# Kernel optimization log

Hardware: AMD Instinct MI355X
Metric: run time of the kernel (lower is better)

The kernel has to match this reference:

```python
import jax, jax.numpy as jnp
import numpy as np

# FP4 E2M1 lookup table: low 3 bits = magnitude code, bit 3 = sign
E2M1_LUT = jnp.array([0.0, 0.5, 1.0, 1.5, 2.0, 3.0, 4.0, 6.0,
                      -0.0, -0.5, -1.0, -1.5, -2.0, -3.0, -4.0, -6.0],
                     dtype=jnp.float32)

INNER_BLOCK = 16    # elements per fp8 (e4m3) inner scale
OUTER_BLOCK = 128   # elements per fp32 outlier scale


def dequant_fp4(w_q, w_os, w_is):
    """Dequantize packed FP4 weights.
    w_q : [out, in//2] int (uint8 semantics: two nibbles per byte)
    w_os: [out, in//128] fp32 outlier scales
    w_is: [out, in//16]  fp32 values on the fp8 e4m3 grid (inner scales)
    returns W: [out, in] fp32
    """
    out_f = w_q.shape[0]
    lo = E2M1_LUT[w_q & 0xF]          # even in-feature indices
    hi = E2M1_LUT[(w_q >> 4) & 0xF]   # odd in-feature indices
    w = jnp.stack([lo, hi], axis=-1).reshape(out_f, -1)  # [out, in]
    w = w * jnp.repeat(w_is, INNER_BLOCK, axis=1)
    w = w * jnp.repeat(w_os, OUTER_BLOCK, axis=1)
    return w


def setup_inputs() -> dict:
    key = jax.random.key(0)
    k1, k2, k3, k4 = jax.random.split(key, 4)
    M, IN, OUT = 8192, 4096, 16384

    x = jax.random.normal(k1, (M, IN), dtype=jnp.float32)

    # packed FP4 codes (uint8 semantics, stored as int32 for portability)
    w_q = jax.random.randint(k2, (OUT, IN // 2), 0, 256, dtype=jnp.int32)

    # per-128-block fp32 outlier scales (positive)
    w_os = jax.random.uniform(k3, (OUT, IN // OUTER_BLOCK), dtype=jnp.float32,
                              minval=0.001, maxval=0.01)

    # per-16-block inner scales, snapped to the fp8 e4m3 grid
    w_is_raw = jax.random.uniform(k4, (OUT, IN // INNER_BLOCK), dtype=jnp.float32,
                                  minval=0.25, maxval=2.0)
    w_is = w_is_raw.astype(jnp.float8_e4m3fn).astype(jnp.float32)

    # transposed dequantized weight, exactly consistent (used by backward)
    w_t = dequant_fp4(w_q, w_os, w_is).T  # [IN, OUT]

    return {"x": x, "w_q": w_q, "w_os": w_os, "w_is": w_is, "w_t": w_t}


def reference(x, w_q, w_os, w_is, w_t):
    # x.float() + flatten-to-2D already satisfied by setup (x is [M, in] fp32).
    w = dequant_fp4(w_q, w_os, w_is)          # [out, in]
    y = jnp.einsum('mk,nk->mn', x, w)         # fused dequant + GEMM math
    return y
```

## Files before the change

kernel.cpp:

```cpp
#include <hip/hip_runtime.h>
#include <hip/hip_bf16.h>
#include <stdint.h>
#include <stddef.h>

#define M_DIM 8192
#define K_DIM 4096
#define N_DIM 16384

#define BM 256
#define BN 256
#define BK 64
#define KT (K_DIM / BK)
#define SLOT_SH (BM * BK)

typedef __attribute__((ext_vector_type(8))) short bf16x8;
typedef __attribute__((ext_vector_type(4))) float f32x4;
typedef __attribute__((ext_vector_type(4))) int   i32x4;

static __device__ __forceinline__ short f2bf(float f) {
    union { float f; uint32_t u; } v; v.f = f;
    uint32_t r = v.u + 0x7FFFu + ((v.u >> 16) & 1u);
    return (short)(r >> 16);
}

static __device__ __forceinline__ float e2m1(int v) {
    int e = (v >> 1) & 3;
    int m = v & 1;
    float mag = (e == 0) ? 0.5f * (float)m
                         : (float)(2 + m) * 0.25f * (float)(1 << e);
    return (v & 8) ? -mag : mag;
}

static __device__ __forceinline__ void gload16(short* lds, const short* g) {
    __builtin_amdgcn_global_load_lds(
        (const __attribute__((address_space(1))) void*)g,
        (__attribute__((address_space(3))) void*)lds,
        16, 0, 0);
}

__global__ void cast_x_kernel(const float* __restrict__ x, short* __restrict__ xb) {
    size_t i = (size_t)blockIdx.x * 256 + threadIdx.x;
    const float4* s = reinterpret_cast<const float4*>(x);
    float4 a = s[2 * i];
    float4 b = s[2 * i + 1];
    bf16x8 o;
    o[0] = f2bf(a.x); o[1] = f2bf(a.y); o[2] = f2bf(a.z); o[3] = f2bf(a.w);
    o[4] = f2bf(b.x); o[5] = f2bf(b.y); o[6] = f2bf(b.z); o[7] = f2bf(b.w);
    reinterpret_cast<bf16x8*>(xb)[i] = o;
}

__global__ void dequant_w_kernel(const int* __restrict__ wq,
                                 const float* __restrict__ wos,
                                 const float* __restrict__ wis,
                                 short* __restrict__ wb) {
    int tid = blockIdx.x * 256 + threadIdx.x;
    int n   = tid >> 8;
    int blk = tid & 255;
    float scale = wis[(n << 8) | blk] * wos[(n << 5) | (blk >> 3)];
    const i32x4* q = reinterpret_cast<const i32x4*>(wq + ((size_t)n << 11) + (blk << 3));
    i32x4 q0 = q[0], q1 = q[1];
    bf16x8 o0, o1;
#pragma unroll
    for (int j = 0; j < 4; ++j) {
        int c = q0[j];
        o0[2 * j]     = f2bf(e2m1(c & 15) * scale);
        o0[2 * j + 1] = f2bf(e2m1((c >> 4) & 15) * scale);
    }
#pragma unroll
    for (int j = 0; j < 4; ++j) {
        int c = q1[j];
        o1[2 * j]     = f2bf(e2m1(c & 15) * scale);
        o1[2 * j + 1] = f2bf(e2m1((c >> 4) & 15) * scale);
    }
    bf16x8* dst = reinterpret_cast<bf16x8*>(wb) + 2 * (size_t)tid;
    dst[0] = o0;
    dst[1] = o1;
}

__global__ __launch_bounds__(512)
void gemm_bt_kernel(const short* __restrict__ A,
                    const short* __restrict__ B,
                    float* __restrict__ C) {
    __shared__ __align__(16) short As[2 * SLOT_SH];
    __shared__ __align__(16) short Bs[2 * SLOT_SH];

    int bid = blockIdx.x;
    int xcd = bid & 7;
    int idx = bid >> 3;
    int im  = idx >> 3;
    int in8 = idx & 7;
    int bm  = im << 8;
    int bn  = ((xcd << 3) + in8) << 8;

    int t    = threadIdx.x;
    int lane = t & 63;
    int w    = t >> 6;
    int wm   = w >> 2;
    int wn   = w & 3;
    int fr   = lane & 15;
    int fq   = lane >> 4;
    int wbase = w << 9;

    int gcol = (((t & 7) ^ ((t >> 3) & 7)) << 3);
    const short* AgB = A + (size_t)(bm + (t >> 3)) * K_DIM + gcol;
    const short* BgB = B + (size_t)(bn + (t >> 3)) * K_DIM + gcol;

    int s0 = fq ^ (fr & 7);
    int s1 = s0 ^ 4;
    int aBase = ((wm << 7) + fr) * 8;
    int bBase = ((wn << 6) + fr) * 8;

    f32x4 acc[8][4] = {};

#define STAGE_A(slot_, kt_)                                                   \
    do {                                                                      \
        const short* _s = AgB + (size_t)(kt_) * BK;                           \
        short* _d = As + (slot_) * SLOT_SH + wbase;                           \
        gload16(_d,         _s);                                              \
        gload16(_d + 4096,  _s + (size_t)64  * K_DIM);                        \
        gload16(_d + 8192,  _s + (size_t)128 * K_DIM);                        \
        gload16(_d + 12288, _s + (size_t)192 * K_DIM);                        \
    } while (0)
#define STAGE_B(slot_, kt_)                                                   \
    do {                                                                      \
        const short* _s = BgB + (size_t)(kt_) * BK;                           \
        short* _d = Bs + (slot_) * SLOT_SH + wbase;                           \
        gload16(_d,         _s);                                              \
        gload16(_d + 4096,  _s + (size_t)64  * K_DIM);                        \
        gload16(_d + 8192,  _s + (size_t)128 * K_DIM);                        \
        gload16(_d + 12288, _s + (size_t)192 * K_DIM);                        \
    } while (0)

#define PHASE_GATE()                                                          \
    do {                                                                      \
        __builtin_amdgcn_sched_barrier(0);                                    \
        __builtin_amdgcn_s_barrier();                                         \
        asm volatile("s_waitcnt lgkmcnt(0)" ::: "memory");                    \
        __builtin_amdgcn_sched_barrier(0);                                    \
    } while (0)

    STAGE_A(0, 0);
    STAGE_B(0, 0);
    asm volatile("s_waitcnt vmcnt(0)" ::: "memory");
    __builtin_amdgcn_s_barrier();

    for (int kt = 0; kt < KT; ++kt) {
        int c     = kt & 1;
        int nslot = c ^ 1;
        int ktn   = (kt + 1) & (KT - 1);
        const bf16x8* Af = reinterpret_cast<const bf16x8*>(As + c * SLOT_SH);
        const bf16x8* Bf = reinterpret_cast<const bf16x8*>(Bs + c * SLOT_SH);

        bf16x8 av[4], aw[4], bv[4];

#pragma unroll
        for (int ni = 0; ni < 4; ++ni) bv[ni] = Bf[bBase + ni * 128 + s0];
#pragma unroll
        for (int mi = 0; mi < 4; ++mi) av[mi] = Af[aBase + mi * 128 + s0];
        STAGE_A(nslot, ktn);
        PHASE_GATE();
        __builtin_amdgcn_s_setprio(1);
#pragma unroll
        for (int mi = 0; mi < 4; ++mi)
#pragma unroll
            for (int ni = 0; ni < 4; ++ni)
                acc[mi][ni] = __builtin_amdgcn_mfma_f32_16x16x32_bf16(
                    av[mi], bv[ni], acc[mi][ni], 0, 0, 0);
        __builtin_amdgcn_s_setprio(0);
        __builtin_amdgcn_s_barrier();

#pragma unroll
        for (int mi = 0; mi < 4; ++mi) aw[mi] = Af[aBase + (mi + 4) * 128 + s0];
        STAGE_B(nslot, ktn);
        PHASE_GATE();
        __builtin_amdgcn_s_setprio(1);
#pragma unroll
        for (int mi = 0; mi < 4; ++mi)
#pragma unroll
            for (int ni = 0; ni < 4; ++ni)
                acc[mi + 4][ni] = __builtin_amdgcn_mfma_f32_16x16x32_bf16(
                    aw[mi], bv[ni], acc[mi + 4][ni], 0, 0, 0);
        __builtin_amdgcn_s_setprio(0);
        __builtin_amdgcn_s_barrier();

#pragma unroll
        for (int ni = 0; ni < 4; ++ni) bv[ni] = Bf[bBase + ni * 128 + s1];
#pragma unroll
        for (int mi = 0; mi < 4; ++mi) av[mi] = Af[aBase + mi * 128 + s1];
        PHASE_GATE();
        __builtin_amdgcn_s_setprio(1);
#pragma unroll
        for (int mi = 0; mi < 4; ++mi)
#pragma unroll
            for (int ni = 0; ni < 4; ++ni)
                acc[mi][ni] = __builtin_amdgcn_mfma_f32_16x16x32_bf16(
                    av[mi], bv[ni], acc[mi][ni], 0, 0, 0);
        __builtin_amdgcn_s_setprio(0);
        __builtin_amdgcn_s_barrier();

#pragma unroll
        for (int mi = 0; mi < 4; ++mi) aw[mi] = Af[aBase + (mi + 4) * 128 + s1];
        PHASE_GATE();
        __builtin_amdgcn_s_setprio(1);
#pragma unroll
        for (int mi = 0; mi < 4; ++mi)
#pragma unroll
            for (int ni = 0; ni < 4; ++ni)
                acc[mi + 4][ni] = __builtin_amdgcn_mfma_f32_16x16x32_bf16(
                    aw[mi], bv[ni], acc[mi + 4][ni], 0, 0, 0);
        __builtin_amdgcn_s_setprio(0);
        asm volatile("s_waitcnt vmcnt(0)" ::: "memory");
        __builtin_amdgcn_s_barrier();
    }
#undef PHASE_GATE
#undef STAGE_A
#undef STAGE_B

#pragma unroll
    for (int mi = 0; mi < 8; ++mi) {
#pragma unroll
        for (int j = 0; j < 4; ++j) {
            size_t row = (size_t)(bm + (wm << 7) + mi * 16 + fq * 4 + j);
            float* Crow = C + row * N_DIM + (bn + (wn << 6) + fr);
#pragma unroll
            for (int ni = 0; ni < 4; ++ni)
                Crow[ni * 16] = acc[mi][ni][j];
        }
    }
}

extern "C" void kernel_launch(void* const* d_in, const int* in_sizes, int n_in,
                              void* d_out, int out_size, void* d_ws, size_t ws_size,
                              hipStream_t stream) {
    const float* x   = (const float*)d_in[0];
    const int*   wq  = (const int*)d_in[1];
    const float* wos = (const float*)d_in[2];
    const float* wis = (const float*)d_in[3];
    float* out = (float*)d_out;

    short* xb = (short*)d_ws;
    short* wb = (short*)((char*)d_ws + (size_t)M_DIM * K_DIM * 2);

    cast_x_kernel<<<(M_DIM * (size_t)K_DIM / 8) / 256, 256, 0, stream>>>(x, xb);
    dequant_w_kernel<<<(N_DIM * (size_t)K_DIM / 16) / 256, 256, 0, stream>>>(wq, wos, wis, wb);
    gemm_bt_kernel<<<(M_DIM / BM) * (N_DIM / BN), 512, 0, stream>>>(xb, wb, out);
}
```

Baseline: 1.227 ms.

## Switch GEMM inner loop from 16x16x32 to 32x32x16 bf16 MFMA tiles

```diff
diff --git a/kernel.cpp b/kernel.cpp
--- a/kernel.cpp
+++ b/kernel.cpp
@@ -15,6 +15,7 @@
 
 typedef __attribute__((ext_vector_type(8))) short bf16x8;
 typedef __attribute__((ext_vector_type(4))) float f32x4;
+typedef __attribute__((ext_vector_type(16))) float f32x16;
 typedef __attribute__((ext_vector_type(4))) int   i32x4;
 
 static __device__ __forceinline__ short f2bf(float f) {
@@ -97,20 +98,24 @@
     int w    = t >> 6;
     int wm   = w >> 2;
     int wn   = w & 3;
-    int fr   = lane & 15;
-    int fq   = lane >> 4;
+    int r31  = lane & 31;
+    int hi   = lane >> 5;
     int wbase = w << 9;
 
     int gcol = (((t & 7) ^ ((t >> 3) & 7)) << 3);
     const short* AgB = A + (size_t)(bm + (t >> 3)) * K_DIM + gcol;
     const short* BgB = B + (size_t)(bn + (t >> 3)) * K_DIM + gcol;
 
-    int s0 = fq ^ (fr & 7);
-    int s1 = s0 ^ 4;
-    int aBase = ((wm << 7) + fr) * 8;
-    int bBase = ((wn << 6) + fr) * 8;
-
-    f32x4 acc[8][4] = {};
+    int sl[4];
+#pragma unroll
+    for (int ks = 0; ks < 4; ++ks) sl[ks] = (ks * 2 + hi) ^ (r31 & 7);
+    int rowA[4], rowB[2];
+#pragma unroll
+    for (int mi = 0; mi < 4; ++mi) rowA[mi] = ((wm << 7) + mi * 32 + r31) * 8;
+#pragma unroll
+    for (int ni = 0; ni < 2; ++ni) rowB[ni] = ((wn << 6) + ni * 32 + r31) * 8;
+
+    f32x16 acc[4][2] = {};
 
 #define STAGE_A(slot_, kt_)                                                   \
     do {                                                                      \
@@ -151,63 +156,55 @@
         const bf16x8* Af = reinterpret_cast<const bf16x8*>(As + c * SLOT_SH);
         const bf16x8* Bf = reinterpret_cast<const bf16x8*>(Bs + c * SLOT_SH);
 
-        bf16x8 av[4], aw[4], bv[4];
-
-#pragma unroll
-        for (int ni = 0; ni < 4; ++ni) bv[ni] = Bf[bBase + ni * 128 + s0];
-#pragma unroll
-        for (int mi = 0; mi < 4; ++mi) av[mi] = Af[aBase + mi * 128 + s0];
+        bf16x8 av[4][2], bv[2][2];
+
+#pragma unroll
+        for (int ni = 0; ni < 2; ++ni) {
+            bv[ni][0] = Bf[rowB[ni] + sl[0]];
+            bv[ni][1] = Bf[rowB[ni] + sl[1]];
+        }
+#pragma unroll
+        for (int mi = 0; mi < 4; ++mi) {
+            av[mi][0] = Af[rowA[mi] + sl[0]];
+            av[mi][1] = Af[rowA[mi] + sl[1]];
+        }
         STAGE_A(nslot, ktn);
         PHASE_GATE();
         __builtin_amdgcn_s_setprio(1);
 #pragma unroll
         for (int mi = 0; mi < 4; ++mi)
 #pragma unroll
-            for (int ni = 0; ni < 4; ++ni)
-                acc[mi][ni] = __builtin_amdgcn_mfma_f32_16x16x32_bf16(
-                    av[mi], bv[ni], acc[mi][ni], 0, 0, 0);
+            for (int ni = 0; ni < 2; ++ni) {
+                acc[mi][ni] = __builtin_amdgcn_mfma_f32_32x32x16_bf16(
+                    av[mi][0], bv[ni][0], acc[mi][ni], 0, 0, 0);
+                acc[mi][ni] = __builtin_amdgcn_mfma_f32_32x32x16_bf16(
+                    av[mi][1], bv[ni][1], acc[mi][ni], 0, 0, 0);
+            }
         __builtin_amdgcn_s_setprio(0);
         __builtin_amdgcn_s_barrier();
 
 #pragma unroll
-        for (int mi = 0; mi < 4; ++mi) aw[mi] = Af[aBase + (mi + 4) * 128 + s0];
+        for (int ni = 0; ni < 2; ++ni) {
+            bv[ni][0] = Bf[rowB[ni] + sl[2]];
+            bv[ni][1] = Bf[rowB[ni] + sl[3]];
+        }
+#pragma unroll
+        for (int mi = 0; mi < 4; ++mi) {
+            av[mi][0] = Af[rowA[mi] + sl[2]];
+            av[mi][1] = Af[rowA[mi] + sl[3]];
+        }
         STAGE_B(nslot, ktn);
         PHASE_GATE();
         __builtin_amdgcn_s_setprio(1);
 #pragma unroll
         for (int mi = 0; mi < 4; ++mi)
 #pragma unroll
-            for (int ni = 0; ni < 4; ++ni)
-                acc[mi + 4][ni] = __builtin_amdgcn_mfma_f32_16x16x32_bf16(
-                    aw[mi], bv[ni], acc[mi + 4][ni], 0, 0, 0);
-        __builtin_amdgcn_s_setprio(0);
-        __builtin_amdgcn_s_barrier();
-
-#pragma unroll
-        for (int ni = 0; ni < 4; ++ni) bv[ni] = Bf[bBase + ni * 128 + s1];
-#pragma unroll
-        for (int mi = 0; mi < 4; ++mi) av[mi] = Af[aBase + mi * 128 + s1];
-        PHASE_GATE();
-        __builtin_amdgcn_s_setprio(1);
-#pragma unroll
-        for (int mi = 0; mi < 4; ++mi)
-#pragma unroll
-            for (int ni = 0; ni < 4; ++ni)
-                acc[mi][ni] = __builtin_amdgcn_mfma_f32_16x16x32_bf16(
-                    av[mi], bv[ni], acc[mi][ni], 0, 0, 0);
-        __builtin_amdgcn_s_setprio(0);
-        __builtin_amdgcn_s_barrier();
-
-#pragma unroll
-        for (int mi = 0; mi < 4; ++mi) aw[mi] = Af[aBase + (mi + 4) * 128 + s1];
-        PHASE_GATE();
-        __builtin_amdgcn_s_setprio(1);
-#pragma unroll
-        for (int mi = 0; mi < 4; ++mi)
-#pragma unroll
-            for (int ni = 0; ni < 4; ++ni)
-                acc[mi + 4][ni] = __builtin_amdgcn_mfma_f32_16x16x32_bf16(
-                    aw[mi], bv[ni], acc[mi + 4][ni], 0, 0, 0);
+            for (int ni = 0; ni < 2; ++ni) {
+                acc[mi][ni] = __builtin_amdgcn_mfma_f32_32x32x16_bf16(
+                    av[mi][0], bv[ni][0], acc[mi][ni], 0, 0, 0);
+                acc[mi][ni] = __builtin_amdgcn_mfma_f32_32x32x16_bf16(
+                    av[mi][1], bv[ni][1], acc[mi][ni], 0, 0, 0);
+            }
         __builtin_amdgcn_s_setprio(0);
         asm volatile("s_waitcnt vmcnt(0)" ::: "memory");
         __builtin_amdgcn_s_barrier();
@@ -217,16 +214,15 @@
 #undef STAGE_B
 
 #pragma unroll
-    for (int mi = 0; mi < 8; ++mi) {
-#pragma unroll
-        for (int j = 0; j < 4; ++j) {
-            size_t row = (size_t)(bm + (wm << 7) + mi * 16 + fq * 4 + j);
-            float* Crow = C + row * N_DIM + (bn + (wn << 6) + fr);
-#pragma unroll
-            for (int ni = 0; ni < 4; ++ni)
-                Crow[ni * 16] = acc[mi][ni][j];
-        }
-    }
+    for (int mi = 0; mi < 4; ++mi)
+#pragma unroll
+        for (int ni = 0; ni < 2; ++ni)
+#pragma unroll
+            for (int r = 0; r < 16; ++r) {
+                size_t row = (size_t)(bm + (wm << 7) + mi * 32 +
+                                      (r & 3) + 8 * (r >> 2) + 4 * hi);
+                C[row * N_DIM + (bn + (wn << 6) + ni * 32 + r31)] = acc[mi][ni][r];
+            }
 }
 
 extern "C" void kernel_launch(void* const* d_in, const int* in_sizes, int n_in,
```

Measured after the change: 1.179 ms. -3.9%, faster.
